# Optimization experiments

Measured on AMD Instinct MI355X. Metric: run time of the kernel, lower is better.

The kernel has to match this reference:

```python
import jax, jax.numpy as jnp
import numpy as np

B, CIN, COUT, H, W = 8, 128, 256, 64, 64
EPS = 1e-5


def conv2d(x, w, b, pad):
    y = jax.lax.conv_general_dilated(
        x, w, window_strides=(1, 1), padding=[(pad, pad), (pad, pad)],
        dimension_numbers=('NCHW', 'OIHW', 'NCHW'))
    return y + b[None, :, None, None]


def deform_sample(x, offset):
    # x: [B,C,H,W], offset: [B,18,H,W] -> sampled: [B,C,9,H,W]
    b, c, h, w = x.shape
    off = offset.reshape(b, 9, 2, h, w)  # (dy, dx) per kernel tap (torchvision v1 order)
    ky = (jnp.arange(9) // 3 - 1).astype(x.dtype)
    kx = (jnp.arange(9) % 3 - 1).astype(x.dtype)
    py = jnp.arange(h, dtype=x.dtype)[None, None, :, None] + ky[None, :, None, None] + off[:, :, 0]
    px = jnp.arange(w, dtype=x.dtype)[None, None, None, :] + kx[None, :, None, None] + off[:, :, 1]
    y0 = jnp.floor(py); x0 = jnp.floor(px)
    fy = py - y0;       fx = px - x0
    xf = x.reshape(b, c, h * w)

    def gather(iy, ix):
        valid = (iy >= 0) & (iy < h) & (ix >= 0) & (ix < w)
        iyc = jnp.clip(iy, 0, h - 1).astype(jnp.int32)
        ixc = jnp.clip(ix, 0, w - 1).astype(jnp.int32)
        idx = (iyc * w + ixc).reshape(b, -1)  # [B, 9*H*W]
        g = jax.vmap(lambda xb, ib: jnp.take(xb, ib, axis=1))(xf, idx)  # [B,C,9HW]
        return g.reshape(b, c, 9, h, w) * valid.astype(x.dtype)[:, None]

    samp = (gather(y0,     x0    ) * ((1 - fy) * (1 - fx))[:, None]
          + gather(y0,     x0 + 1) * ((1 - fy) * fx      )[:, None]
          + gather(y0 + 1, x0    ) * (fy * (1 - fx)      )[:, None]
          + gather(y0 + 1, x0 + 1) * (fy * fx            )[:, None])
    return samp


def setup_inputs():
    key = jax.random.key(0)
    ks = jax.random.split(key, 8)
    return {
        'x':     jax.random.normal(ks[0], (B, CIN, H, W), jnp.float32),
        'w_off': jax.random.normal(ks[1], (18, CIN, 3, 3), jnp.float32) * 0.01,
        'b_off': jnp.zeros((18,), jnp.float32),
        'w_def': jax.random.normal(ks[2], (COUT, CIN, 3, 3), jnp.float32) * 0.03,
        'b_def': jax.random.normal(ks[3], (COUT,), jnp.float32) * 0.01,
        'gamma': jnp.ones((COUT,), jnp.float32),
        'beta':  jnp.zeros((COUT,), jnp.float32),
        'w_sc':  jax.random.normal(ks[4], (COUT, CIN, 1, 1), jnp.float32) * 0.05,
        'b_sc':  jnp.zeros((COUT,), jnp.float32),
    }


def reference(x, w_off, b_off, w_def, b_def, gamma, beta, w_sc, b_sc):
    offset = conv2d(x, w_off, b_off, pad=1)                 # [B,18,H,W]
    samp = deform_sample(x, offset)                         # [B,C,9,H,W]
    out = jnp.einsum('bckhw,ock->bohw', samp, w_def.reshape(COUT, CIN, 9))
    out = out + b_def[None, :, None, None]
    # BatchNorm2d (training mode: batch statistics)
    mean = out.mean(axis=(0, 2, 3))
    var = out.var(axis=(0, 2, 3))
    out = (out - mean[None, :, None, None]) * jax.lax.rsqrt(var + EPS)[None, :, None, None]
    out = out * gamma[None, :, None, None] + beta[None, :, None, None]
    out = out + conv2d(x, w_sc, b_sc, pad=0)                # residual shortcut (1x1)
    return jax.nn.relu(out)
```

## Files before the change

### kernel.cpp

```cpp
#include <hip/hip_runtime.h>

typedef __attribute__((ext_vector_type(8))) short bf16x8;
typedef __attribute__((ext_vector_type(4))) float f32x4;

__device__ __forceinline__ float bf2f(unsigned short u) {
  return __uint_as_float(((unsigned int)u) << 16);
}
__device__ __forceinline__ unsigned short f2bf(float f) {
  unsigned int u = __float_as_uint(f);
  u += 0x7fffu + ((u >> 16) & 1u);
  return (unsigned short)(u >> 16);
}

constexpr size_t OFF_XPAD = 0;
constexpr size_t SZ_XPAD  = (size_t)8 * 66 * 66 * 128 * 2;
constexpr size_t OFF_WB   = OFF_XPAD + SZ_XPAD;
constexpr size_t SZ_WB    = (size_t)9 * 16 * 256 * 8 * 2;
constexpr size_t OFF_WS2  = OFF_WB + SZ_WB;
constexpr size_t SZ_WS2   = (size_t)16 * 256 * 8 * 2;
constexpr size_t OFF_WO   = OFF_WS2 + SZ_WS2;
constexpr size_t SZ_WO    = (size_t)9 * 16 * 32 * 8 * 2;
constexpr size_t OFF_YM   = OFF_WO + SZ_WO;
constexpr size_t SZ_YM    = (size_t)512 * 512 * 32 * 2;
constexpr size_t OFF_SR   = OFF_YM + SZ_YM;
constexpr size_t SZ_SR    = (size_t)8 * 256 * 2 * 4;


__global__ __launch_bounds__(256) void k_prep(const float* __restrict__ x,
                                              unsigned short* __restrict__ xp,
                                              const float* __restrict__ wdef,
                                              const float* __restrict__ wsc,
                                              const float* __restrict__ woff,
                                              unsigned short* __restrict__ wB,
                                              unsigned short* __restrict__ wS,
                                              unsigned short* __restrict__ wO,
                                              float* __restrict__ statsRaw) {
  int t = threadIdx.x;
  if (blockIdx.x == 690) {
    for (int i = t; i < 4096; i += 256) statsRaw[i] = 0.f;
    return;
  }
  if (blockIdx.x >= 512) {
    int base = ((blockIdx.x - 512) * 256 + t) * 8;
    unsigned short w8[8];
    if (base < 294912) {
      int n = (base >> 3) & 255, kb = (base >> 11) & 15, tap = base >> 15;
#pragma unroll
      for (int j = 0; j < 8; ++j)
        w8[j] = f2bf(wdef[((size_t)n * 128 + kb * 8 + j) * 9 + tap]);
      *(bf16x8*)(wB + base) = *(const bf16x8*)w8;
    } else if (base < 327680) {
      int i0 = base - 294912;
      int n = (i0 >> 3) & 255, kb = i0 >> 11;
#pragma unroll
      for (int j = 0; j < 8; ++j)
        w8[j] = f2bf(wsc[(size_t)n * 128 + kb * 8 + j]);
      *(bf16x8*)(wS + i0) = *(const bf16x8*)w8;
    } else {
      int i0 = base - 327680;
      int n = (i0 >> 3) & 31, kb = (i0 >> 8) & 15, tap = i0 >> 12;
#pragma unroll
      for (int j = 0; j < 8; ++j)
        w8[j] = f2bf(n < 18 ? woff[((size_t)n * 128 + kb * 8 + j) * 9 + tap] : 0.f);
      *(bf16x8*)(wO + i0) = *(const bf16x8*)w8;
    }
    return;
  }
  int blk = blockIdx.x;
  int b = blk & 7, h = blk >> 3;
  __shared__ unsigned short xt[128 * 68];
  {
    unsigned short* base = xp + (size_t)b * 66 * 66 * 128;
    ushort4 z4 = {0, 0, 0, 0};
    if (t < 64) {
      int col = (t >> 5) ? 65 : 0;
      int i = t & 31;
      *(ushort4*)(base + ((size_t)(h + 1) * 66 + col) * 128 + i * 4) = z4;
    }
    if (h == 0) {
      for (int i = t; i < 2112; i += 256) {
        *(ushort4*)(base + (size_t)i * 4) = z4;
        *(ushort4*)(base + (size_t)65 * 66 * 128 + (size_t)i * 4) = z4;
      }
    }
  }
  {
#pragma unroll
    for (int i4 = 0; i4 < 8; ++i4) {
      int idx = t + i4 * 256;
      int row = idx >> 4, col = (idx & 15) * 4;
      float4 f = *(const float4*)&x[(((size_t)b * 128 + row) * 64 + h) * 64 + col];
      ushort4 u4;
      u4.x = f2bf(f.x); u4.y = f2bf(f.y); u4.z = f2bf(f.z); u4.w = f2bf(f.w);
      *(ushort4*)&xt[row * 68 + col] = u4;
    }
  }
  __syncthreads();
  {
    int w = t & 63, cg = t >> 6;
    unsigned short tmp[32];
#pragma unroll
    for (int i = 0; i < 32; ++i) tmp[i] = xt[(cg * 32 + i) * 68 + w];
    unsigned short* dst = xp + ((size_t)(b * 66 + h + 1) * 66 + (w + 1)) * 128 + cg * 32;
#pragma unroll
    for (int i8 = 0; i8 < 4; ++i8)
      *(bf16x8*)(dst + i8 * 8) = *(const bf16x8*)&tmp[i8 * 8];
  }
}

__global__ __launch_bounds__(512, 4) void k_main(const unsigned short* __restrict__ xp,
                                                 const unsigned short* __restrict__ wB,
                                                 const unsigned short* __restrict__ wO,
                                                 const float* __restrict__ boff,
                                                 const float* __restrict__ bdef,
                                                 unsigned short* __restrict__ ymain,
                                                 float* __restrict__ statsRaw) {
  int blk = blockIdx.x;
  int b = blk & 7, h = blk >> 3;
  int t = threadIdx.x;
  int lane = t & 63, wid = t >> 6;
  int m = lane & 15, quad = lane >> 4;
  __shared__ __align__(16) unsigned short At[2][64 * 136];
  __shared__ float offsL[9][64][2];

  if (wid < 4) {
    f32x4 a0 = {0.f, 0.f, 0.f, 0.f}, a1 = {0.f, 0.f, 0.f, 0.f};
    int px = wid * 16 + m;
    const unsigned short* xbase = xp + ((size_t)(b * 66 + h) * 66 + px) * 128 + quad * 8;
    for (int tap = 0; tap < 9; ++tap) {
      const unsigned short* arow = xbase + ((tap / 3) * 66 + (tap % 3)) * 128;
#pragma unroll
      for (int kk = 0; kk < 4; ++kk) {
        bf16x8 a = *(const bf16x8*)(arow + kk * 32);
        const unsigned short* bb = wO + (size_t)(tap * 16 + kk * 4 + quad) * 256;
        bf16x8 b0 = *(const bf16x8*)(bb + m * 8);
        bf16x8 b1 = *(const bf16x8*)(bb + (16 + m) * 8);
        a0 = __builtin_amdgcn_mfma_f32_16x16x32_bf16(a, b0, a0, 0, 0, 0);
        a1 = __builtin_amdgcn_mfma_f32_16x16x32_bf16(a, b1, a1, 0, 0, 0);
      }
    }
#pragma unroll
    for (int r = 0; r < 4; ++r) {
      int pxs = wid * 16 + quad * 4 + r;
      offsL[m >> 1][pxs][m & 1] = a0[r] + boff[m];
      if (m < 2) offsL[8][pxs][m] = a1[r] + boff[16 + m];
    }
  }

  f32x4 acc[4][2];
#pragma unroll
  for (int i = 0; i < 4; ++i)
#pragma unroll
    for (int j = 0; j < 2; ++j) acc[i][j] = (f32x4){0.f, 0.f, 0.f, 0.f};

  int px_s = t >> 3, sub = t & 7;
  const unsigned short* xb_base = xp + (size_t)b * 66 * 66 * 128;
  int nb = wid * 32;

  bf16x8 Breg[4][2];
  auto loadB = [&](int tap) {
#pragma unroll
    for (int kk = 0; kk < 4; ++kk)
#pragma unroll
      for (int ns = 0; ns < 2; ++ns)
        Breg[kk][ns] = *(const bf16x8*)(wB + ((size_t)(tap * 16 + kk * 4 + quad) * 256 + nb + ns * 16 + m) * 8);
  };

  auto sample_prep = [&](int tap, float* wgt, const unsigned short** p) {
    float2 ov = *(const float2*)&offsL[tap][px_s][0];
    int ky = tap / 3 - 1, kx = tap % 3 - 1;
    float py = (float)(h + ky) + ov.x;
    float pxf = (float)(px_s + kx) + ov.y;
    float y0f = floorf(py), x0f = floorf(pxf);
    float fy = py - y0f, fx = pxf - x0f;
    int iy0 = (int)y0f, ix0 = (int)x0f;
#pragma unroll
    for (int j = 0; j < 4; ++j) {
      int iy = iy0 + (j >> 1), ix = ix0 + (j & 1);
      float wy = (j >> 1) ? fy : 1.f - fy;
      float wx = (j & 1) ? fx : 1.f - fx;
      bool valid = (iy >= 0) && (iy < 64) && (ix >= 0) && (ix < 64);
      int iyc = min(max(iy, 0), 63), ixc = min(max(ix, 0), 63);
      wgt[j] = valid ? wy * wx : 0.f;
      p[j] = xb_base + ((size_t)(iyc + 1) * 66 + (ixc + 1)) * 128 + sub * 8;
    }
  };
  auto load_g1 = [&](const unsigned short** p, int g, bf16x8* v) {
#pragma unroll
    for (int j = 0; j < 4; ++j)
      v[j] = *(const bf16x8*)(p[j] + g * 64);
  };
  auto store_g1 = [&](unsigned short* dst, int g, const float* wgt, bf16x8* v) {
    bf16x8 o;
#pragma unroll
    for (int j = 0; j < 8; ++j) {
      float s = fmaf(wgt[0], bf2f((unsigned short)v[0][j]),
                fmaf(wgt[1], bf2f((unsigned short)v[1][j]),
                fmaf(wgt[2], bf2f((unsigned short)v[2][j]),
                     wgt[3] * bf2f((unsigned short)v[3][j]))));
      o[j] = (short)f2bf(s);
    }
    *(bf16x8*)(dst + g * 64) = o;
  };
  auto mfma_half = [&](const unsigned short* buf, int kk0) {
#pragma unroll
    for (int kk = kk0; kk < kk0 + 2; ++kk) {
      bf16x8 af[4];
#pragma unroll
      for (int ms = 0; ms < 4; ++ms)
        af[ms] = *(const bf16x8*)(buf + (ms * 16 + m) * 136 + kk * 32 + quad * 8);
#pragma unroll
      for (int ns = 0; ns < 2; ++ns)
#pragma unroll
        for (int ms = 0; ms < 4; ++ms)
          acc[ms][ns] = __builtin_amdgcn_mfma_f32_16x16x32_bf16(af[ms], Breg[kk][ns], acc[ms][ns], 0, 0, 0);
    }
  };

  loadB(0);
  __syncthreads();
  {
    float wgt[4]; const unsigned short* p[4]; bf16x8 v0[4], v1[4];
    sample_prep(0, wgt, p);
    unsigned short* dst = &At[0][px_s * 136 + sub * 8];
    load_g1(p, 0, v0); load_g1(p, 1, v1);
    store_g1(dst, 0, wgt, v0); store_g1(dst, 1, wgt, v1);
  }
#pragma unroll
  for (int tap = 0; tap < 9; ++tap) {
    __syncthreads();
    const unsigned short* cur = At[tap & 1];
    unsigned short* dst = &At[(tap + 1) & 1][px_s * 136 + sub * 8];
    if (tap < 8) {
      float wgt[4]; const unsigned short* p[4]; bf16x8 v0[4], v1[4];
      sample_prep(tap + 1, wgt, p);
      load_g1(p, 0, v0);
      load_g1(p, 1, v1);
      mfma_half(cur, 0);
      store_g1(dst, 0, wgt, v0);
      mfma_half(cur, 2);
      loadB(tap + 1);
      store_g1(dst, 1, wgt, v1);
    } else {
      mfma_half(cur, 0);
      mfma_half(cur, 2);
    }
  }

#pragma unroll
  for (int ns = 0; ns < 2; ++ns) {
    int n = nb + ns * 16 + m;
    float bias = bdef[n];
    float s = 0.f, q = 0.f;
#pragma unroll
    for (int ms = 0; ms < 4; ++ms)
#pragma unroll
      for (int r = 0; r < 4; ++r) {
        float v = acc[ms][ns][r] + bias;
        acc[ms][ns][r] = v;
        s += v;
        q += v * v;
      }
    s += __shfl_xor(s, 16); s += __shfl_xor(s, 32);
    q += __shfl_xor(q, 16); q += __shfl_xor(q, 32);
    if (quad == 0) {
      atomicAdd(&statsRaw[((size_t)b * 256 + n) * 2 + 0], s);
      atomicAdd(&statsRaw[((size_t)b * 256 + n) * 2 + 1], q);
    }
  }
  {
    unsigned short yfrag[32];
#pragma unroll
    for (int ns = 0; ns < 2; ++ns)
#pragma unroll
      for (int ms = 0; ms < 4; ++ms)
#pragma unroll
        for (int r = 0; r < 4; ++r)
          yfrag[ns * 16 + ms * 4 + r] = f2bf(acc[ms][ns][r]);
    unsigned short* dst = ymain + (size_t)blk * 16384 + t * 8;
#pragma unroll
    for (int k = 0; k < 4; ++k)
      *(bf16x8*)(dst + k * 4096) = *(const bf16x8*)&yfrag[k * 8];
  }
}

__global__ __launch_bounds__(512, 4) void k_final(const unsigned short* __restrict__ xp,
                                                  const unsigned short* __restrict__ wS,
                                                  const unsigned short* __restrict__ ymain,
                                                  const float* __restrict__ statsRaw,
                                                  const float* __restrict__ gamma,
                                                  const float* __restrict__ beta,
                                                  const float* __restrict__ bsc,
                                                  float* __restrict__ out) {
  int blk = blockIdx.x;
  int b = blk & 7, h = blk >> 3;
  int t = threadIdx.x;
  int lane = t & 63, wid = t >> 6;
  int m = lane & 15, quad = lane >> 4;
  __shared__ __align__(16) float tr[128 * 68];
  __shared__ float sAB[512];
  if (t < 256) {
    float s = 0.f, q = 0.f;
#pragma unroll
    for (int i = 0; i < 8; ++i) {
      float2 pq = *(const float2*)&statsRaw[((size_t)i * 256 + t) * 2];
      s += pq.x;
      q += pq.y;
    }
    float mean = s * (1.f / 32768.f);
    float var = q * (1.f / 32768.f) - mean * mean;
    float inv = rsqrtf(var + 1e-5f);
    float A = gamma[t] * inv;
    sAB[t] = A;
    sAB[256 + t] = beta[t] - mean * A;
  }
  f32x4 accS[4][2];
#pragma unroll
  for (int i = 0; i < 4; ++i)
#pragma unroll
    for (int j = 0; j < 2; ++j) accS[i][j] = (f32x4){0.f, 0.f, 0.f, 0.f};
  const unsigned short* xrow = xp + ((size_t)(b * 66 + h + 1) * 66 + 1) * 128;
  int nb = wid * 32;
#pragma unroll
  for (int kk = 0; kk < 4; ++kk) {
    bf16x8 af[4];
#pragma unroll
    for (int ms = 0; ms < 4; ++ms)
      af[ms] = *(const bf16x8*)(xrow + (ms * 16 + m) * 128 + kk * 32 + quad * 8);
#pragma unroll
    for (int ns = 0; ns < 2; ++ns) {
      bf16x8 bfr = *(const bf16x8*)(wS + ((size_t)(kk * 4 + quad) * 256 + nb + ns * 16 + m) * 8);
#pragma unroll
      for (int ms = 0; ms < 4; ++ms)
        accS[ms][ns] = __builtin_amdgcn_mfma_f32_16x16x32_bf16(af[ms], bfr, accS[ms][ns], 0, 0, 0);
    }
  }
  bf16x8 yf[4];
  {
    const unsigned short* ysrc = ymain + (size_t)blk * 16384 + t * 8;
#pragma unroll
    for (int k = 0; k < 4; ++k)
      yf[k] = *(const bf16x8*)(ysrc + k * 4096);
  }
  __syncthreads();
  int pass_own = wid >> 2;
  for (int pass = 0; pass < 2; ++pass) {
    if (pass_own == pass) {
#pragma unroll
      for (int ns = 0; ns < 2; ++ns) {
        int n = nb + ns * 16 + m;
        float A = sAB[n], Bc = sAB[256 + n], bs = bsc[n];
        int nl = n - pass * 128;
#pragma unroll
        for (int ms = 0; ms < 4; ++ms)
#pragma unroll
          for (int r = 0; r < 4; ++r) {
            int e = ns * 16 + ms * 4 + r;
            float y = bf2f((unsigned short)yf[e >> 3][e & 7]);
            float v = fmaf(y, A, Bc) + accS[ms][ns][r] + bs;
            tr[nl * 68 + ms * 16 + quad * 4 + r] = fmaxf(v, 0.f);
          }
      }
    }
    __syncthreads();
    {
      int nl = t >> 2, q4 = t & 3;
      float* orow = out + ((size_t)(b * 256 + pass * 128 + nl) * 64 + h) * 64 + q4 * 16;
      const float* lrow = &tr[nl * 68 + q4 * 16];
#pragma unroll
      for (int i4 = 0; i4 < 4; ++i4)
        *(f32x4*)(orow + i4 * 4) = *(const f32x4*)(lrow + i4 * 4);
    }
    __syncthreads();
  }
}

extern "C" void kernel_launch(void* const* d_in, const int* in_sizes, int n_in,
                              void* d_out, int out_size, void* d_ws, size_t ws_size,
                              hipStream_t stream) {
  const float* x     = (const float*)d_in[0];
  const float* w_off = (const float*)d_in[1];
  const float* b_off = (const float*)d_in[2];
  const float* w_def = (const float*)d_in[3];
  const float* b_def = (const float*)d_in[4];
  const float* gamma = (const float*)d_in[5];
  const float* beta  = (const float*)d_in[6];
  const float* w_sc  = (const float*)d_in[7];
  const float* b_sc  = (const float*)d_in[8];
  float* out = (float*)d_out;

  char* ws = (char*)d_ws;
  unsigned short* xpad  = (unsigned short*)(ws + OFF_XPAD);
  unsigned short* wB    = (unsigned short*)(ws + OFF_WB);
  unsigned short* wS    = (unsigned short*)(ws + OFF_WS2);
  unsigned short* wO    = (unsigned short*)(ws + OFF_WO);
  unsigned short* ymain = (unsigned short*)(ws + OFF_YM);
  float* statsRaw       = (float*)(ws + OFF_SR);

  k_prep<<<691, 256, 0, stream>>>(x, xpad, w_def, w_sc, w_off, wB, wS, wO, statsRaw);
  k_main<<<512, 512, 0, stream>>>(xpad, wB, wO, b_off, b_def, ymain, statsRaw);
  k_final<<<512, 512, 0, stream>>>(xpad, wS, ymain, statsRaw, gamma, beta, b_sc, out);
}
```

Measured before the change: 155.9 us.

## Move shortcut 1x1 conv into main kernel and make final pass elementwise NCHW

The 1x1 shortcut GEMM moves from the final kernel into k_main. k_main now writes both the deformable-conv output and the shortcut result as bf16 in NCHW layout, transposed through shared memory and written with nontemporal stores. The final kernel becomes a simple per-channel BN-apply, add and ReLU over contiguous rows, one block per (b, channel). The A-tile LDS stride also changes from 136 to 140. In exchange the shortcut is stored as an extra bf16 intermediate (more HBM traffic and a rounding step), and k_main uses more LDS and registers, which may lower occupancy.

```diff
diff --git a/kernel.cpp b/kernel.cpp
--- a/kernel.cpp
+++ b/kernel.cpp
@@ -21,8 +21,10 @@
 constexpr size_t OFF_WO   = OFF_WS2 + SZ_WS2;
 constexpr size_t SZ_WO    = (size_t)9 * 16 * 32 * 8 * 2;
 constexpr size_t OFF_YM   = OFF_WO + SZ_WO;
-constexpr size_t SZ_YM    = (size_t)512 * 512 * 32 * 2;
-constexpr size_t OFF_SR   = OFF_YM + SZ_YM;
+constexpr size_t SZ_YM    = (size_t)8 * 256 * 4096 * 2;
+constexpr size_t OFF_SC   = OFF_YM + SZ_YM;
+constexpr size_t SZ_SC    = SZ_YM;
+constexpr size_t OFF_SR   = OFF_SC + SZ_SC;
 constexpr size_t SZ_SR    = (size_t)8 * 256 * 2 * 4;
 
 
@@ -111,16 +113,20 @@
 __global__ __launch_bounds__(512, 4) void k_main(const unsigned short* __restrict__ xp,
                                                  const unsigned short* __restrict__ wB,
                                                  const unsigned short* __restrict__ wO,
+                                                 const unsigned short* __restrict__ wS,
                                                  const float* __restrict__ boff,
                                                  const float* __restrict__ bdef,
-                                                 unsigned short* __restrict__ ymain,
+                                                 const float* __restrict__ bsc,
+                                                 unsigned short* __restrict__ ynchw,
+                                                 unsigned short* __restrict__ scnchw,
                                                  float* __restrict__ statsRaw) {
   int blk = blockIdx.x;
   int b = blk & 7, h = blk >> 3;
   int t = threadIdx.x;
   int lane = t & 63, wid = t >> 6;
   int m = lane & 15, quad = lane >> 4;
-  __shared__ __align__(16) unsigned short At[2][64 * 136];
+  __shared__ __align__(16) unsigned short At[2][64 * 140];
+  __shared__ __align__(16) unsigned short ytr[256 * 72];
   __shared__ float offsL[9][64][2];
 
   if (wid < 4) {
@@ -208,7 +214,7 @@
       bf16x8 af[4];
 #pragma unroll
       for (int ms = 0; ms < 4; ++ms)
-        af[ms] = *(const bf16x8*)(buf + (ms * 16 + m) * 136 + kk * 32 + quad * 8);
+        af[ms] = *(const bf16x8*)(buf + (ms * 16 + m) * 140 + kk * 32 + quad * 8);
 #pragma unroll
       for (int ns = 0; ns < 2; ++ns)
 #pragma unroll
@@ -222,7 +228,7 @@
   {
     float wgt[4]; const unsigned short* p[4]; bf16x8 v0[4], v1[4];
     sample_prep(0, wgt, p);
-    unsigned short* dst = &At[0][px_s * 136 + sub * 8];
+    unsigned short* dst = &At[0][px_s * 140 + sub * 8];
     load_g1(p, 0, v0); load_g1(p, 1, v1);
     store_g1(dst, 0, wgt, v0); store_g1(dst, 1, wgt, v1);
   }
@@ -230,7 +236,7 @@
   for (int tap = 0; tap < 9; ++tap) {
     __syncthreads();
     const unsigned short* cur = At[tap & 1];
-    unsigned short* dst = &At[(tap + 1) & 1][px_s * 136 + sub * 8];
+    unsigned short* dst = &At[(tap + 1) & 1][px_s * 140 + sub * 8];
     if (tap < 8) {
       float wgt[4]; const unsigned short* p[4]; bf16x8 v0[4], v1[4];
       sample_prep(tap + 1, wgt, p);
@@ -268,110 +274,115 @@
       atomicAdd(&statsRaw[((size_t)b * 256 + n) * 2 + 1], q);
     }
   }
-  {
-    unsigned short yfrag[32];
-#pragma unroll
-    for (int ns = 0; ns < 2; ++ns)
+
+  f32x4 accS[4][2];
+#pragma unroll
+  for (int i = 0; i < 4; ++i)
+#pragma unroll
+    for (int j = 0; j < 2; ++j) accS[i][j] = (f32x4){0.f, 0.f, 0.f, 0.f};
+  {
+    const unsigned short* xrow = xp + ((size_t)(b * 66 + h + 1) * 66 + 1) * 128;
+#pragma unroll
+    for (int kk = 0; kk < 4; ++kk) {
+      bf16x8 af[4];
 #pragma unroll
       for (int ms = 0; ms < 4; ++ms)
-#pragma unroll
-        for (int r = 0; r < 4; ++r)
-          yfrag[ns * 16 + ms * 4 + r] = f2bf(acc[ms][ns][r]);
-    unsigned short* dst = ymain + (size_t)blk * 16384 + t * 8;
-#pragma unroll
-    for (int k = 0; k < 4; ++k)
-      *(bf16x8*)(dst + k * 4096) = *(const bf16x8*)&yfrag[k * 8];
-  }
-}
-
-__global__ __launch_bounds__(512, 4) void k_final(const unsigned short* __restrict__ xp,
-                                                  const unsigned short* __restrict__ wS,
-                                                  const unsigned short* __restrict__ ymain,
-                                                  const float* __restrict__ statsRaw,
-                                                  const float* __restrict__ gamma,
-                                                  const float* __restrict__ beta,
-                                                  const float* __restrict__ bsc,
-                                                  float* __restrict__ out) {
+        af[ms] = *(const bf16x8*)(xrow + (ms * 16 + m) * 128 + kk * 32 + quad * 8);
+#pragma unroll
+      for (int ns = 0; ns < 2; ++ns) {
+        bf16x8 bfr = *(const bf16x8*)(wS + ((size_t)(kk * 4 + quad) * 256 + nb + ns * 16 + m) * 8);
+#pragma unroll
+        for (int ms = 0; ms < 4; ++ms)
+          accS[ms][ns] = __builtin_amdgcn_mfma_f32_16x16x32_bf16(af[ms], bfr, accS[ms][ns], 0, 0, 0);
+      }
+    }
+  }
+
+  __syncthreads();
+  {
+#pragma unroll
+    for (int ns = 0; ns < 2; ++ns) {
+      int n = nb + ns * 16 + m;
+#pragma unroll
+      for (int ms = 0; ms < 4; ++ms) {
+        unsigned short y4[4];
+#pragma unroll
+        for (int r = 0; r < 4; ++r) y4[r] = f2bf(acc[ms][ns][r]);
+        *(ushort4*)&ytr[n * 72 + ms * 16 + quad * 4] = *(const ushort4*)y4;
+      }
+    }
+  }
+  __syncthreads();
+  {
+    int n = t >> 1, half = t & 1;
+    const unsigned short* lrow = ytr + n * 72 + half * 32;
+    unsigned short* grow = ynchw + ((size_t)(b * 256 + n) << 12) + h * 64 + half * 32;
+#pragma unroll
+    for (int i = 0; i < 4; ++i)
+      __builtin_nontemporal_store(*(const bf16x8*)(lrow + i * 8), (bf16x8*)(grow + i * 8));
+  }
+  __syncthreads();
+  {
+#pragma unroll
+    for (int ns = 0; ns < 2; ++ns) {
+      int n = nb + ns * 16 + m;
+      float bs = bsc[n];
+#pragma unroll
+      for (int ms = 0; ms < 4; ++ms) {
+        unsigned short s4[4];
+#pragma unroll
+        for (int r = 0; r < 4; ++r) s4[r] = f2bf(accS[ms][ns][r] + bs);
+        *(ushort4*)&ytr[n * 72 + ms * 16 + quad * 4] = *(const ushort4*)s4;
+      }
+    }
+  }
+  __syncthreads();
+  {
+    int n = t >> 1, half = t & 1;
+    const unsigned short* lrow = ytr + n * 72 + half * 32;
+    unsigned short* grow = scnchw + ((size_t)(b * 256 + n) << 12) + h * 64 + half * 32;
+#pragma unroll
+    for (int i = 0; i < 4; ++i)
+      __builtin_nontemporal_store(*(const bf16x8*)(lrow + i * 8), (bf16x8*)(grow + i * 8));
+  }
+}
+
+__global__ __launch_bounds__(256) void k_final(const unsigned short* __restrict__ ynchw,
+                                               const unsigned short* __restrict__ scnchw,
+                                               const float* __restrict__ statsRaw,
+                                               const float* __restrict__ gamma,
+                                               const float* __restrict__ beta,
+                                               float* __restrict__ out) {
   int blk = blockIdx.x;
-  int b = blk & 7, h = blk >> 3;
+  int b = blk & 7, n = blk >> 3;
   int t = threadIdx.x;
-  int lane = t & 63, wid = t >> 6;
-  int m = lane & 15, quad = lane >> 4;
-  __shared__ __align__(16) float tr[128 * 68];
-  __shared__ float sAB[512];
-  if (t < 256) {
-    float s = 0.f, q = 0.f;
-#pragma unroll
-    for (int i = 0; i < 8; ++i) {
-      float2 pq = *(const float2*)&statsRaw[((size_t)i * 256 + t) * 2];
-      s += pq.x;
-      q += pq.y;
-    }
-    float mean = s * (1.f / 32768.f);
-    float var = q * (1.f / 32768.f) - mean * mean;
-    float inv = rsqrtf(var + 1e-5f);
-    float A = gamma[t] * inv;
-    sAB[t] = A;
-    sAB[256 + t] = beta[t] - mean * A;
-  }
-  f32x4 accS[4][2];
-#pragma unroll
-  for (int i = 0; i < 4; ++i)
-#pragma unroll
-    for (int j = 0; j < 2; ++j) accS[i][j] = (f32x4){0.f, 0.f, 0.f, 0.f};
-  const unsigned short* xrow = xp + ((size_t)(b * 66 + h + 1) * 66 + 1) * 128;
-  int nb = wid * 32;
-#pragma unroll
-  for (int kk = 0; kk < 4; ++kk) {
-    bf16x8 af[4];
-#pragma unroll
-    for (int ms = 0; ms < 4; ++ms)
-      af[ms] = *(const bf16x8*)(xrow + (ms * 16 + m) * 128 + kk * 32 + quad * 8);
-#pragma unroll
-    for (int ns = 0; ns < 2; ++ns) {
-      bf16x8 bfr = *(const bf16x8*)(wS + ((size_t)(kk * 4 + quad) * 256 + nb + ns * 16 + m) * 8);
-#pragma unroll
-      for (int ms = 0; ms < 4; ++ms)
-        accS[ms][ns] = __builtin_amdgcn_mfma_f32_16x16x32_bf16(af[ms], bfr, accS[ms][ns], 0, 0, 0);
-    }
-  }
-  bf16x8 yf[4];
-  {
-    const unsigned short* ysrc = ymain + (size_t)blk * 16384 + t * 8;
-#pragma unroll
-    for (int k = 0; k < 4; ++k)
-      yf[k] = *(const bf16x8*)(ysrc + k * 4096);
-  }
-  __syncthreads();
-  int pass_own = wid >> 2;
-  for (int pass = 0; pass < 2; ++pass) {
-    if (pass_own == pass) {
-#pragma unroll
-      for (int ns = 0; ns < 2; ++ns) {
-        int n = nb + ns * 16 + m;
-        float A = sAB[n], Bc = sAB[256 + n], bs = bsc[n];
-        int nl = n - pass * 128;
-#pragma unroll
-        for (int ms = 0; ms < 4; ++ms)
-#pragma unroll
-          for (int r = 0; r < 4; ++r) {
-            int e = ns * 16 + ms * 4 + r;
-            float y = bf2f((unsigned short)yf[e >> 3][e & 7]);
-            float v = fmaf(y, A, Bc) + accS[ms][ns][r] + bs;
-            tr[nl * 68 + ms * 16 + quad * 4 + r] = fmaxf(v, 0.f);
-          }
-      }
-    }
-    __syncthreads();
-    {
-      int nl = t >> 2, q4 = t & 3;
-      float* orow = out + ((size_t)(b * 256 + pass * 128 + nl) * 64 + h) * 64 + q4 * 16;
-      const float* lrow = &tr[nl * 68 + q4 * 16];
-#pragma unroll
-      for (int i4 = 0; i4 < 4; ++i4)
-        *(f32x4*)(orow + i4 * 4) = *(const f32x4*)(lrow + i4 * 4);
-    }
-    __syncthreads();
+  float s = 0.f, q = 0.f;
+#pragma unroll
+  for (int i = 0; i < 8; ++i) {
+    float2 pq = *(const float2*)&statsRaw[((size_t)i * 256 + n) * 2];
+    s += pq.x;
+    q += pq.y;
+  }
+  float mean = s * (1.f / 32768.f);
+  float var = q * (1.f / 32768.f) - mean * mean;
+  float A = gamma[n] * rsqrtf(var + 1e-5f);
+  float Bc = beta[n] - mean * A;
+  size_t base = ((size_t)(b * 256 + n) << 12) + t * 16;
+  const unsigned short* yp = ynchw + base;
+  const unsigned short* sp = scnchw + base;
+  float* op = out + base;
+#pragma unroll
+  for (int g = 0; g < 2; ++g) {
+    bf16x8 yv = *(const bf16x8*)(yp + g * 8);
+    bf16x8 sv = *(const bf16x8*)(sp + g * 8);
+    f32x4 o0, o1;
+#pragma unroll
+    for (int j = 0; j < 4; ++j) {
+      o0[j] = fmaxf(fmaf(bf2f((unsigned short)yv[j]), A, Bc) + bf2f((unsigned short)sv[j]), 0.f);
+      o1[j] = fmaxf(fmaf(bf2f((unsigned short)yv[4 + j]), A, Bc) + bf2f((unsigned short)sv[4 + j]), 0.f);
+    }
+    *(f32x4*)(op + g * 8 + 0) = o0;
+    *(f32x4*)(op + g * 8 + 4) = o1;
   }
 }
 
@@ -394,10 +405,11 @@
   unsigned short* wB    = (unsigned short*)(ws + OFF_WB);
   unsigned short* wS    = (unsigned short*)(ws + OFF_WS2);
   unsigned short* wO    = (unsigned short*)(ws + OFF_WO);
-  unsigned short* ymain = (unsigned short*)(ws + OFF_YM);
+  unsigned short* ynchw = (unsigned short*)(ws + OFF_YM);
+  unsigned short* scnch = (unsigned short*)(ws + OFF_SC);
   float* statsRaw       = (float*)(ws + OFF_SR);
 
   k_prep<<<691, 256, 0, stream>>>(x, xpad, w_def, w_sc, w_off, wB, wS, wO, statsRaw);
-  k_main<<<512, 512, 0, stream>>>(xpad, wB, wO, b_off, b_def, ymain, statsRaw);
-  k_final<<<512, 512, 0, stream>>>(xpad, wS, ymain, statsRaw, gamma, beta, b_sc, out);
-}
+  k_main<<<512, 512, 0, stream>>>(xpad, wB, wO, wS, b_off, b_def, b_sc, ynchw, scnch, statsRaw);
+  k_final<<<2048, 256, 0, stream>>>(ynchw, scnch, statsRaw, gamma, beta, out);
+}
```

Measured after the change: 225.6 us. 44.7% more time.
